# Kernel tuning notes

Measured on AMD Instinct MI355X. Metric: run time of the kernel, lower is better.

## Reference

```python
import jax, jax.numpy as jnp
import numpy as np

N = 30000
E = 480000
F = 256
H = 32
HEADS = 4
NUM_LABEL = 6
NEG_SLOPE = 0.2
BN_EPS = 1e-5
NUM_ITER = 3
ROUTE_NODES = 2 * (HEADS + HEADS)  # 16
PC_OUT = 8


def squash(t, axis=-1):
    sq = (t ** 2).sum(axis=axis, keepdims=True)
    return (sq / (1.0 + sq)) * t / jnp.sqrt(sq)


def glorot(key, shape):
    fan_in, fan_out = shape[-2], shape[-1]
    s = jnp.sqrt(6.0 / (fan_in + fan_out))
    return jax.random.uniform(key, shape, jnp.float32, -s, s)


def setup_inputs() -> dict:
    key = jax.random.key(0)
    ks = jax.random.split(key, 10)
    x = jax.random.normal(ks[0], (N, F), jnp.float32)
    rng = np.random.default_rng(0)
    src = rng.integers(0, N, E)
    dst = rng.integers(0, N, E)
    dst = np.where(src == dst, (dst + 1) % N, dst)  # no self loops (torch code removes them)
    edge_index = jnp.asarray(np.stack([src, dst]), jnp.int32)
    y = jax.random.randint(ks[1], (N,), 0, NUM_LABEL, jnp.int32)
    return {
        'x': x,
        'gamma': jnp.ones((F,), jnp.float32),
        'beta': jnp.zeros((F,), jnp.float32),
        'W_lin': glorot(ks[2], (F, HEADS * H)),
        'b_lin': jnp.zeros((HEADS * H,), jnp.float32),
        'W_gat': glorot(ks[3], (F, HEADS * H)),
        'att': glorot(ks[4], (1, HEADS, 2 * H)),
        'b_gat': jnp.zeros((HEADS * H,), jnp.float32),
        'Wp': glorot(ks[5], (2, H, PC_OUT)),
        'bp': jnp.zeros((2, PC_OUT), jnp.float32),
        'route_w': jax.random.normal(ks[6], (NUM_LABEL, ROUTE_NODES, PC_OUT, H), jnp.float32),
        'edge_index': edge_index,
        'y': y,
    }


def _forward(x, gamma, beta, W_lin, b_lin, W_gat, att, b_gat, Wp, bp, route_w, edge_index, y):
    n = x.shape[0]
    # BatchNorm1d (training-mode batch statistics, biased variance)
    mean = x.mean(axis=0)
    var = ((x - mean) ** 2).mean(axis=0)
    xb = (x - mean) / jnp.sqrt(var + BN_EPS) * gamma + beta

    hidden = (xb @ W_lin + b_lin).reshape(n, HEADS, H)

    # ---- GATConv (concat=True, add self-loops) ----
    xt = (xb @ W_gat).reshape(n, HEADS, H)
    loop = jnp.arange(n, dtype=edge_index.dtype)
    src = jnp.concatenate([edge_index[0], loop])
    dst = jnp.concatenate([edge_index[1], loop])
    x_i = xt[dst]  # [Et, HEADS, H] target
    x_j = xt[src]  # [Et, HEADS, H] source
    a_i, a_j = att[:, :, :H], att[:, :, H:]
    alpha = (x_i * a_i).sum(-1) + (x_j * a_j).sum(-1)  # [Et, HEADS]
    alpha = jnp.where(alpha >= 0, alpha, NEG_SLOPE * alpha)
    amax = jax.ops.segment_max(alpha, dst, num_segments=n)
    e = jnp.exp(alpha - amax[dst])
    denom = jax.ops.segment_sum(e, dst, num_segments=n)
    alpha = e / (denom[dst] + 1e-16)
    msg = x_j * alpha[:, :, None]
    aggr = jax.ops.segment_sum(msg, dst, num_segments=n)  # [n, HEADS, H]
    gat_out = aggr.reshape(n, HEADS * H) + b_gat

    xc = jnp.concatenate([gat_out.reshape(n, HEADS, H), hidden], axis=1)  # [n, 2*HEADS, H]
    xc = jax.nn.relu(xc)

    # ---- primary capsules: 2 Linear(H->8), cat on route axis, squash ----
    pc = jnp.einsum('nrh,cho->ncro', xc, Wp) + bp[None, :, None, :]  # [n,2,8,8]
    u = squash(pc.reshape(n, ROUTE_NODES, PC_OUT))  # [n,16,8]

    # ---- digit capsules: dynamic routing (softmax over route nodes, dim=2) ----
    priors = jnp.einsum('nri,crio->cnro', u, route_w)  # [6,n,16,H]
    logits = jnp.zeros(priors.shape[:3], priors.dtype)  # [6,n,16]
    for it in range(NUM_ITER):
        probs = jax.nn.softmax(logits, axis=2)
        v = squash((probs[..., None] * priors).sum(axis=2))  # [6,n,H]
        if it != NUM_ITER - 1:
            logits = logits + (priors * v[:, :, None, :]).sum(-1)

    xo = v.transpose(1, 0, 2)  # [n,6,H]
    features = xo.reshape(n, NUM_LABEL * H)
    output = jnp.sqrt((xo ** 2).sum(-1))  # [n,6] capsule lengths
    logp = jax.nn.log_softmax(output, axis=-1)
    loss = -jnp.take_along_axis(logp, y[:, None].astype(jnp.int32), axis=1).mean()
    return output, loss, features


def reference(x, gamma, beta, W_lin, b_lin, W_gat, att, b_gat, Wp, bp, route_w, edge_index, y):
    return _forward(x, gamma, beta, W_lin, b_lin, W_gat, att, b_gat, Wp, bp, route_w, edge_index, y)
```

## Files before the change

kernel.cpp:

```cpp
#include <hip/hip_runtime.h>
#include <hip/hip_bf16.h>

#define NND 30000
#define NE  480000
#define FD  256
#define HD  32
#define HEADS 4
#define NLAB 6
#define NEG_SLOPE 0.2f
#define BN_EPS 1e-5f
#define LOG2E 1.44269504f

#define WS_FLAG      0
#define WS_BNSUM     4
#define WS_BNSQ      260
#define WS_LOSS      516
#define WS_COUNTS    520
#define WS_ZERO_ELEMS 30524
#define WS_OFFSETS   30524
#define WS_CURSOR    60528
#define WS_GAMMA     90528
#define WS_BETA      90784
#define WS_WLIN      91040
#define WS_BLIN      123808
#define WS_WGAT      123936
#define WS_ATT       156704
#define WS_BGAT      156960
#define WS_WP        157088
#define WS_BP        157600
#define WS_RW        157616
#define WS_SCALE     182192
#define WS_SHIFT     182448
#define WS_WC        182704
#define WS_BC        248240
#define WS_SD        248496
#define WS_SS        368496
#define WS_ONORM     488496
#define WS_CSR       668496
#define WS_XF        1178496
#define WS_U         1178496
#define WS_BLKSUM    5018496
#define WS_BLKOFF    5018624
#define WS_Y         8858496
#define WS_XCG       16538496

#define OUT_LOSS_IDX 180000
#define OUT_FEAT_IDX 180001

#define SCAN_NB 118

typedef float v2f __attribute__((ext_vector_type(2)));

__device__ __forceinline__ float lrelu(float a) { return a >= 0.0f ? a : NEG_SLOPE * a; }

#if __has_builtin(__builtin_amdgcn_rcpf)
__device__ __forceinline__ float frcp(float x) { return __builtin_amdgcn_rcpf(x); }
#else
__device__ __forceinline__ float frcp(float x) { return 1.0f / x; }
#endif
#if __has_builtin(__builtin_amdgcn_sqrtf)
__device__ __forceinline__ float fsqrt(float x) { return __builtin_amdgcn_sqrtf(x); }
#else
__device__ __forceinline__ float fsqrt(float x) { return sqrtf(x); }
#endif
#if __has_builtin(__builtin_amdgcn_exp2f)
__device__ __forceinline__ float fexp2(float x) { return __builtin_amdgcn_exp2f(x); }
#else
__device__ __forceinline__ float fexp2(float x) { return exp2f(x); }
#endif

__device__ __forceinline__ int get_flag(const unsigned int* graw) {
    return ((graw[0] & 0xFFFFu) == 0x3F80u) ? 1 : 0;
}

__device__ __forceinline__ float bf2f(unsigned short h) {
    return __uint_as_float(((unsigned int)h) << 16);
}

__device__ __forceinline__ void pin(float& x) { asm volatile("" : "+v"(x)); }

template<int CTRL>
__device__ __forceinline__ float fdpp(float v) {
    return __int_as_float(__builtin_amdgcn_mov_dpp(__float_as_int(v), CTRL, 0xF, 0xF, true));
}
template<int PAT>
__device__ __forceinline__ float fswz(float v) {
    return __int_as_float(__builtin_amdgcn_ds_swizzle(__float_as_int(v), PAT));
}
__device__ __forceinline__ float redq(float v) {
    v += fdpp<0xB1>(v);
    v += fdpp<0x4E>(v);
    v += fswz<0x101F>(v);
    v += fswz<0x201F>(v);
    v += fswz<0x401F>(v);
    return v;
}
__device__ __forceinline__ float redq_sum64(float v) {
    v = redq(v);
    return v + __shfl_xor(v, 32);
}
__device__ __forceinline__ float redq_max64(float v) {
    v = fmaxf(v, fdpp<0xB1>(v));
    v = fmaxf(v, fdpp<0x4E>(v));
    v = fmaxf(v, fswz<0x101F>(v));
    v = fmaxf(v, fswz<0x201F>(v));
    v = fmaxf(v, fswz<0x401F>(v));
    return fmaxf(v, __shfl_xor(v, 32));
}
__device__ __forceinline__ void dreduce(float dp[8], int k, float out[8]) {
    #pragma unroll
    for (int j = 0; j < 8; ++j) {
        dp[j] += fdpp<0xB1>(dp[j]);
        dp[j] += fdpp<0x4E>(dp[j]);
    }
    float A = (k == 0) ? dp[0] : (k == 1) ? dp[1] : (k == 2) ? dp[2] : dp[3];
    float B = (k == 0) ? dp[4] : (k == 1) ? dp[5] : (k == 2) ? dp[6] : dp[7];
    A += fswz<0x101F>(A); A += fswz<0x201F>(A); A += fswz<0x401F>(A);
    B += fswz<0x101F>(B); B += fswz<0x201F>(B); B += fswz<0x401F>(B);
    out[0] = fdpp<0x00>(A); out[1] = fdpp<0x55>(A); out[2] = fdpp<0xAA>(A); out[3] = fdpp<0xFF>(A);
    out[4] = fdpp<0x00>(B); out[5] = fdpp<0x55>(B); out[6] = fdpp<0xAA>(B); out[7] = fdpp<0xFF>(B);
}

__device__ __forceinline__ float cvt_load(const void* p, int i, int f) {
    if (f) return __bfloat162float(((const __hip_bfloat16*)p)[i]);
    return ((const float*)p)[i];
}

#define CVT_XBLK 2048
__global__ void k_convert_all(const void* src, float* xdst,
                              const void* p0, const void* p1, const void* p2, const void* p3,
                              const void* p4, const void* p5, const void* p6, const void* p7,
                              const void* p8, const void* p9, float* pdst) {
    int f = get_flag((const unsigned int*)p0);
    if (blockIdx.x < CVT_XBLK) {
        const int nquad = NND * FD / 4;
        for (int q = blockIdx.x * blockDim.x + threadIdx.x; q < nquad; q += CVT_XBLK * blockDim.x) {
            float4 o;
            if (f) {
                ushort4 hv = ((const ushort4*)src)[q];
                o.x = bf2f(hv.x); o.y = bf2f(hv.y);
                o.z = bf2f(hv.z); o.w = bf2f(hv.w);
            } else {
                o = ((const float4*)src)[q];
            }
            ((float4*)xdst)[q] = o;
        }
        return;
    }
    int i = (blockIdx.x - CVT_XBLK) * blockDim.x + threadIdx.x;
    if (i >= 91664) return;
    const void* p; int off;
    if      (i < 256)   { p = p0; off = i; }
    else if (i < 512)   { p = p1; off = i - 256; }
    else if (i < 33280) { p = p2; off = i - 512; }
    else if (i < 33408) { p = p3; off = i - 33280; }
    else if (i < 66176) { p = p4; off = i - 33408; }
    else if (i < 66432) { p = p5; off = i - 66176; }
    else if (i < 66560) { p = p6; off = i - 66432; }
    else if (i < 67072) { p = p7; off = i - 66560; }
    else if (i < 67088) { p = p8; off = i - 67072; }
    else                { p = p9; off = i - 67088; }
    pdst[i] = cvt_load(p, off, f);
}

#define BN_NB 960
__global__ void k_bn_stats(const float* xf, float* bn_sum, float* bn_sq) {
    int t = threadIdx.x;
    int rows = (NND + gridDim.x - 1) / gridDim.x;
    int r0 = blockIdx.x * rows;
    int r1 = min(NND, r0 + rows);
    float s = 0.0f, ss = 0.0f;
    for (int r = r0; r < r1; ++r) {
        float v = xf[(size_t)r * FD + t];
        s += v; ss += v * v;
    }
    atomicAdd(&bn_sum[t], s);
    atomicAdd(&bn_sq[t], ss);
}

__global__ void k_fold(const float* bn_sum, const float* bn_sq, const float* gamma,
                       const float* beta, const float* wlin, const float* wgat,
                       const float* blin, float* Wc, float* bc) {
    int j = blockIdx.x;
    int k = threadIdx.x;
    float mean = bn_sum[k] / (float)NND;
    float var  = bn_sq[k] / (float)NND - mean * mean;
    float inv  = 1.0f / sqrtf(var + BN_EPS);
    float sc   = gamma[k] * inv;
    float sh   = beta[k] - mean * sc;
    float w = (j < 128) ? wlin[k * 128 + j] : wgat[k * 128 + (j - 128)];
    Wc[k * 256 + j] = sc * w;
    __shared__ float red[256];
    red[k] = sh * w;
    __syncthreads();
    for (int s = 128; s > 0; s >>= 1) { if (k < s) red[k] += red[k + s]; __syncthreads(); }
    if (k == 0) bc[j] = red[0] + (j < 128 ? blin[j] : 0.0f);
}

__global__ __launch_bounds__(256) void k_gemm(const float* A, const float* B,
                                              const float* bias, float* C) {
    __shared__ __align__(16) float As[16][128];
    __shared__ __align__(16) float Bs[16][64];
    int t  = threadIdx.x;
    int bm = blockIdx.x * 128;
    int bn = blockIdx.y * 64;
    int tr = t / 16, tc = t % 16;
    v2f acc[8][2] = {};
    int alm = t >> 2;
    int alk = (t & 3) * 4;
    int blk = t >> 4;
    int bln = (t & 15) * 4;
    for (int k0 = 0; k0 < 256; k0 += 16) {
        #pragma unroll
        for (int half = 0; half < 2; ++half) {
            int row = bm + alm + half * 64;
            float4 av = make_float4(0.f, 0.f, 0.f, 0.f);
            if (row < NND) av = *(const float4*)(A + (size_t)row * 256 + k0 + alk);
            int m = alm + half * 64;
            As[alk + 0][m] = av.x; As[alk + 1][m] = av.y;
            As[alk + 2][m] = av.z; As[alk + 3][m] = av.w;
        }
        float4 bv = *(const float4*)(B + (size_t)(k0 + blk) * 256 + bn + bln);
        *(float4*)&Bs[blk][bln] = bv;
        __syncthreads();
        #pragma unroll
        for (int kk = 0; kk < 16; ++kk) {
            float a[8];
            *(float4*)&a[0] = *(const float4*)&As[kk][tr * 8];
            *(float4*)&a[4] = *(const float4*)&As[kk][tr * 8 + 4];
            float4 b4 = *(const float4*)&Bs[kk][tc * 4];
            v2f b0; b0.x = b4.x; b0.y = b4.y;
            v2f b1; b1.x = b4.z; b1.y = b4.w;
            #pragma unroll
            for (int i = 0; i < 8; ++i) {
                v2f av; av.x = a[i]; av.y = a[i];
                acc[i][0] += av * b0;
                acc[i][1] += av * b1;
            }
        }
        __syncthreads();
    }
    #pragma unroll
    for (int i = 0; i < 8; ++i) {
        int row = bm + tr * 8 + i;
        if (row < NND) {
            int col = bn + tc * 4;
            float4 o;
            o.x = acc[i][0].x + bias[col + 0];
            o.y = acc[i][0].y + bias[col + 1];
            o.z = acc[i][1].x + bias[col + 2];
            o.w = acc[i][1].y + bias[col + 3];
            *(float4*)(C + (size_t)row * 256 + col) = o;
        }
    }
}

__global__ void k_scores(const float* Y, const float* attf, float* sD, float* sS) {
    int idx = blockIdx.x * blockDim.x + threadIdx.x;
    if (idx >= NND * HEADS) return;
    int n = idx >> 2, h = idx & 3;
    const float4* xr = (const float4*)(Y + (size_t)n * 256 + 128 + h * 32);
    const float4* ai = (const float4*)(attf + h * 64);
    const float4* aj = (const float4*)(attf + h * 64 + 32);
    float si = 0.f, sj = 0.f;
    #pragma unroll
    for (int k = 0; k < 8; ++k) {
        float4 x = xr[k], a = ai[k], b = aj[k];
        si += x.x*a.x + x.y*a.y + x.z*a.z + x.w*a.w;
        sj += x.x*b.x + x.y*b.y + x.z*b.z + x.w*b.w;
    }
    sD[idx] = si * LOG2E; sS[idx] = sj * LOG2E;
}

__global__ void k_count(const int* ei, int* counts) {
    int e = blockIdx.x * blockDim.x + threadIdx.x;
    if (e >= NE + NND) return;
    int d = (e < NE) ? ei[NE + e] : (e - NE);
    atomicAdd(&counts[d], 1);
}

__global__ void k_scan_blk(const int* counts, int* offsets, int* blksum) {
    int t = threadIdx.x, b = blockIdx.x;
    int i = b * 256 + t;
    int v = (i < NND) ? counts[i] : 0;
    int lane = t & 63, wv = t >> 6;
    int x = v;
    #pragma unroll
    for (int off = 1; off < 64; off <<= 1) {
        int y = __shfl_up(x, off);
        if (lane >= off) x += y;
    }
    __shared__ int wsum[4];
    if (lane == 63) wsum[wv] = x;
    __syncthreads();
    int add = 0;
    #pragma unroll
    for (int w = 0; w < 4; ++w) add += (w < wv) ? wsum[w] : 0;
    if (i < NND) offsets[i] = add + x - v;
    if (t == 255) blksum[b] = add + x;
}

__global__ void k_scan_add(const int* blksum, int* offsets, int* cursor) {
    int t = threadIdx.x, b = blockIdx.x;
    __shared__ int red[256];
    red[t] = (t < SCAN_NB && t < b) ? blksum[t] : 0;
    __syncthreads();
    for (int s = 128; s > 0; s >>= 1) { if (t < s) red[t] += red[t + s]; __syncthreads(); }
    int add = red[0];
    int i = b * 256 + t;
    if (i >= NND) return;
    int o = offsets[i] + add;
    offsets[i] = o;
    cursor[i] = o;
}

__global__ void k_scatter(const int* ei, int* cursor, int* csr) {
    int e = blockIdx.x * blockDim.x + threadIdx.x;
    if (e >= NE + NND) return;
    int s, d;
    if (e < NE) { s = ei[e]; d = ei[NE + e]; } else { s = d = e - NE; }
    int pos = atomicAdd(&cursor[d], 1);
    csr[pos] = s;
}

__global__ __launch_bounds__(256) void k_aggr(const float* Y, const float* sD, const float* sS,
                                              const int* offsets, const int* counts, const int* csr,
                                              const float* bgat, float* xcg) {
    int wave = (blockIdx.x * blockDim.x + threadIdx.x) >> 6;
    int lane = threadIdx.x & 63;
    if (wave >= NND) return;
    int n = wave;
    int start = offsets[n], deg = counts[n];
    float4 sd = *(const float4*)(sD + (size_t)n * 4);
    int hA = lane >> 5;
    float m0 = -1e30f, m1 = -1e30f, m2 = -1e30f, m3 = -1e30f;
    float d0 = 0.f, d1 = 0.f, d2 = 0.f, d3 = 0.f;
    float acc0 = 0.f, acc1 = 0.f;
    for (int base = 0; base < deg; base += 64) {
        int cnt = min(64, deg - base);
        int sidx = 0;
        float a0 = -1e30f, a1 = -1e30f, a2 = -1e30f, a3 = -1e30f;
        if (base + lane < deg) {
            sidx = csr[start + base + lane];
            float4 sj = *(const float4*)(sS + (size_t)sidx * 4);
            a0 = lrelu(sd.x + sj.x);
            a1 = lrelu(sd.y + sj.y);
            a2 = lrelu(sd.z + sj.z);
            a3 = lrelu(sd.w + sj.w);
        }
        float nm0 = fmaxf(m0, redq_max64(a0));
        float nm1 = fmaxf(m1, redq_max64(a1));
        float nm2 = fmaxf(m2, redq_max64(a2));
        float nm3 = fmaxf(m3, redq_max64(a3));
        if (base) {
            float s0 = fexp2(m0 - nm0), s1 = fexp2(m1 - nm1);
            float s2 = fexp2(m2 - nm2), s3 = fexp2(m3 - nm3);
            d0 *= s0; d1 *= s1; d2 *= s2; d3 *= s3;
            acc0 *= hA ? s1 : s0;
            acc1 *= hA ? s3 : s2;
        }
        m0 = nm0; m1 = nm1; m2 = nm2; m3 = nm3;
        float w0 = 0.f, w1 = 0.f, w2 = 0.f, w3 = 0.f;
        if (base + lane < deg) {
            w0 = fexp2(a0 - m0); w1 = fexp2(a1 - m1);
            w2 = fexp2(a2 - m2); w3 = fexp2(a3 - m3);
        }
        d0 += w0; d1 += w1; d2 += w2; d3 += w3;
        for (int j = 0; j < cnt; ++j) {
            int s2i = __builtin_amdgcn_readlane(sidx, j);
            float wa0 = __int_as_float(__builtin_amdgcn_readlane(__float_as_int(w0), j));
            float wa1 = __int_as_float(__builtin_amdgcn_readlane(__float_as_int(w1), j));
            float wb0 = __int_as_float(__builtin_amdgcn_readlane(__float_as_int(w2), j));
            float wb1 = __int_as_float(__builtin_amdgcn_readlane(__float_as_int(w3), j));
            float wA = hA ? wa1 : wa0;
            float wB = hA ? wb1 : wb0;
            const float* xrow = Y + (size_t)s2i * 256 + 128;
            acc0 += wA * xrow[lane];
            acc1 += wB * xrow[64 + lane];
        }
    }
    d0 = redq_sum64(d0); d1 = redq_sum64(d1);
    d2 = redq_sum64(d2); d3 = redq_sum64(d3);
    float i0 = frcp(d0 + 1e-16f), i1 = frcp(d1 + 1e-16f);
    float i2 = frcp(d2 + 1e-16f), i3 = frcp(d3 + 1e-16f);
    float iA = hA ? i1 : i0;
    float iB = hA ? i3 : i2;
    float r0 = acc0 * iA + bgat[lane];
    float r1 = acc1 * iB + bgat[64 + lane];
    xcg[(size_t)n * 128 + lane]      = r0 > 0.f ? r0 : 0.f;
    xcg[(size_t)n * 128 + 64 + lane] = r1 > 0.f ? r1 : 0.f;
}

__global__ __launch_bounds__(256, 4) void k_u(const float* Y, const float* xcg,
                                              const float* Wpf, const float* bpf, float* uG) {
    int lane = threadIdx.x & 63;
    int gw = blockIdx.x * 4 + (threadIdx.x >> 6);
    int nwaves = gridDim.x * 4;
    int r = lane >> 3, oo = lane & 7;
    float wpA[32], wpB[32];
    #pragma unroll
    for (int k = 0; k < 32; ++k) {
        wpA[k] = Wpf[k * 8 + oo];
        wpB[k] = Wpf[256 + k * 8 + oo];
    }
    #pragma unroll
    for (int k = 0; k < 32; ++k) { pin(wpA[k]); pin(wpB[k]); }
    float bpA = bpf[oo], bpB = bpf[8 + oo];
    for (int n = gw; n < NND; n += nwaves) {
        const float* rowp = (r < 4) ? (xcg + (size_t)n * 128 + r * 32)
                                    : (Y + (size_t)n * 256 + (r - 4) * 32);
        float pcA = bpA, pcB = bpB;
        #pragma unroll
        for (int k4 = 0; k4 < 8; ++k4) {
            float4 xv = *(const float4*)(rowp + k4 * 4);
            xv.x = fmaxf(xv.x, 0.f); xv.y = fmaxf(xv.y, 0.f);
            xv.z = fmaxf(xv.z, 0.f); xv.w = fmaxf(xv.w, 0.f);
            pcA += xv.x * wpA[k4*4+0] + xv.y * wpA[k4*4+1] + xv.z * wpA[k4*4+2] + xv.w * wpA[k4*4+3];
            pcB += xv.x * wpB[k4*4+0] + xv.y * wpB[k4*4+1] + xv.z * wpB[k4*4+2] + xv.w * wpB[k4*4+3];
        }
        float sA = pcA * pcA, sB = pcB * pcB;
        sA += fdpp<0xB1>(sA); sA += fdpp<0x4E>(sA); sA += fswz<0x101F>(sA);
        sB += fdpp<0xB1>(sB); sB += fdpp<0x4E>(sB); sB += fswz<0x101F>(sB);
        float cA = fsqrt(sA) * frcp(1.0f + sA);
        float cB = fsqrt(sB) * frcp(1.0f + sB);
        uG[(size_t)n * 128 + lane]      = pcA * cA;
        uG[(size_t)n * 128 + 64 + lane] = pcB * cB;
    }
}

__global__ __launch_bounds__(256, 3) void k_route3(const float* uG, const float* rwf,
                                                   float* onorm, void* dout,
                                                   const unsigned int* graw) {
    int flag = get_flag(graw);
    int t = threadIdx.x;
    int lane = t & 63;
    int nwg = gridDim.x;
    int swz = (blockIdx.x & 7) * (nwg >> 3) + (blockIdx.x >> 3);
    int c = swz % 6;
    int wv = t >> 6;
    int widx = (swz / 6) * 4 + wv;
    int nstep = (nwg / 6) * 4;
    int h = lane >> 5, o = lane & 31;
    int k = lane & 3;
    float rw[8][8];
    #pragma unroll
    for (int j = 0; j < 8; ++j)
        #pragma unroll
        for (int i = 0; i < 8; ++i)
            rw[j][i] = rwf[(((c * 16) + (h * 8 + j)) * 8 + i) * 32 + o];
    #pragma unroll
    for (int j = 0; j < 8; ++j)
        #pragma unroll
        for (int i = 0; i < 8; ++i)
            pin(rw[j][i]);
    float* outf = (float*)dout;
    __hip_bfloat16* outb = (__hip_bfloat16*)dout;
    for (int n = widx; n < NND; n += nstep) {
        const float* up = uG + (size_t)n * 128 + h * 64;
        float p[8];
        #pragma unroll
        for (int j = 0; j < 8; ++j) {
            float4 a = *(const float4*)(up + j * 8);
            float4 b = *(const float4*)(up + j * 8 + 4);
            p[j] = a.x*rw[j][0] + a.y*rw[j][1] + a.z*rw[j][2] + a.w*rw[j][3]
                 + b.x*rw[j][4] + b.y*rw[j][5] + b.z*rw[j][6] + b.w*rw[j][7];
        }
        float tl = p[0]+p[1]+p[2]+p[3]+p[4]+p[5]+p[6]+p[7];
        float s = (tl + __shfl_xor(tl, 32)) * 0.0625f;
        float sq = redq(s * s);
        float v = s * (fsqrt(sq) * frcp(1.0f + sq));
        float vs = v * LOG2E;
        float logits[8], dp[8];
        #pragma unroll
        for (int j = 0; j < 8; ++j) dp[j] = p[j] * vs;
        dreduce(dp, k, logits);
        float sq3 = 0.f, v3 = 0.f;
        #pragma unroll
        for (int it = 0; it < 2; ++it) {
            float m01 = fmaxf(logits[0], logits[1]);
            float m23 = fmaxf(logits[2], logits[3]);
            float m45 = fmaxf(logits[4], logits[5]);
            float m67 = fmaxf(logits[6], logits[7]);
            float mx = fmaxf(fmaxf(m01, m23), fmaxf(m45, m67));
            mx = fmaxf(mx, __shfl_xor(mx, 32));
            float e[8]; float se = 0.f;
            #pragma unroll
            for (int j = 0; j < 8; ++j) { e[j] = fexp2(logits[j] - mx); se += e[j]; }
            se += __shfl_xor(se, 32);
            float inv = frcp(se);
            float sl = 0.f;
            #pragma unroll
            for (int j = 0; j < 8; ++j) sl += e[j] * p[j];
            sl *= inv;
            float ss = sl + __shfl_xor(sl, 32);
            float q = redq(ss * ss);
            float vv = ss * (fsqrt(q) * frcp(1.0f + q));
            if (it == 0) {
                float dd[8], lu[8];
                float vvs = vv * LOG2E;
                #pragma unroll
                for (int j = 0; j < 8; ++j) dd[j] = p[j] * vvs;
                dreduce(dd, k, lu);
                #pragma unroll
                for (int j = 0; j < 8; ++j) logits[j] += lu[j];
            } else { v3 = vv; sq3 = q; }
        }
        if (lane < 32) {
            size_t fidx = (size_t)OUT_FEAT_IDX + (size_t)n * 192 + c * 32 + o;
            if (flag) outb[fidx] = __float2bfloat16(v3); else outf[fidx] = v3;
            if (lane == 0) {
                float norm = sq3 * frcp(1.0f + sq3);
                onorm[n * 6 + c] = norm;
                size_t oidx = (size_t)n * 6 + c;
                if (flag) outb[oidx] = __float2bfloat16(norm); else outf[oidx] = norm;
            }
        }
    }
}

__global__ void k_loss(const float* onorm, const int* y, float* acc) {
    float l = 0.f;
    for (int n = blockIdx.x * blockDim.x + threadIdx.x; n < NND; n += gridDim.x * blockDim.x) {
        const float* v = onorm + n * 6;
        float m = v[0];
        #pragma unroll
        for (int cc = 1; cc < 6; ++cc) m = fmaxf(m, v[cc]);
        float s = 0.f;
        #pragma unroll
        for (int cc = 0; cc < 6; ++cc) s += __expf(v[cc] - m);
        l += m + __logf(s) - v[y[n]];
    }
    __shared__ float red[256];
    red[threadIdx.x] = l;
    __syncthreads();
    for (int s = 128; s > 0; s >>= 1) { if (threadIdx.x < s) red[threadIdx.x] += red[threadIdx.x + s]; __syncthreads(); }
    if (threadIdx.x == 0) atomicAdd(acc, red[0]);
}

__global__ void k_loss_fin(const float* acc, void* dout, const unsigned int* graw) {
    float v = acc[0] / (float)NND;
    if (get_flag(graw)) ((__hip_bfloat16*)dout)[OUT_LOSS_IDX] = __float2bfloat16(v);
    else                ((float*)dout)[OUT_LOSS_IDX] = v;
}

extern "C" void kernel_launch(void* const* d_in, const int* in_sizes, int n_in,
                              void* d_out, int out_size, void* d_ws, size_t ws_size,
                              hipStream_t stream) {
    (void)in_sizes; (void)n_in; (void)out_size; (void)ws_size;
    float* ws = (float*)d_ws;
    int*  wsi = (int*)d_ws;
    const int* ei = (const int*)d_in[11];
    const int* y  = (const int*)d_in[12];
    const unsigned int* graw = (const unsigned int*)d_in[1];

    hipMemsetAsync(d_ws, 0, (size_t)WS_ZERO_ELEMS * 4, stream);

    k_convert_all<<<CVT_XBLK + (91664 + 255) / 256, 256, 0, stream>>>(
        d_in[0], ws + WS_XF,
        d_in[1], d_in[2], d_in[3], d_in[4], d_in[5], d_in[6], d_in[7], d_in[8], d_in[9], d_in[10],
        ws + WS_GAMMA);

    k_bn_stats<<<BN_NB, 256, 0, stream>>>(ws + WS_XF, ws + WS_BNSUM, ws + WS_BNSQ);
    k_fold<<<256, 256, 0, stream>>>(ws + WS_BNSUM, ws + WS_BNSQ, ws + WS_GAMMA, ws + WS_BETA,
                                    ws + WS_WLIN, ws + WS_WGAT, ws + WS_BLIN,
                                    ws + WS_WC, ws + WS_BC);

    k_gemm<<<dim3((NND + 127) / 128, 4), 256, 0, stream>>>(ws + WS_XF, ws + WS_WC, ws + WS_BC, ws + WS_Y);

    k_scores<<<(NND * HEADS + 255) / 256, 256, 0, stream>>>(ws + WS_Y, ws + WS_ATT, ws + WS_SD, ws + WS_SS);

    k_count<<<(NE + NND + 255) / 256, 256, 0, stream>>>(ei, wsi + WS_COUNTS);
    k_scan_blk<<<SCAN_NB, 256, 0, stream>>>(wsi + WS_COUNTS, wsi + WS_OFFSETS, wsi + WS_BLKSUM);
    k_scan_add<<<SCAN_NB, 256, 0, stream>>>(wsi + WS_BLKSUM, wsi + WS_OFFSETS, wsi + WS_CURSOR);
    k_scatter<<<(NE + NND + 255) / 256, 256, 0, stream>>>(ei, wsi + WS_CURSOR, wsi + WS_CSR);

    k_aggr<<<(NND + 3) / 4, 256, 0, stream>>>(ws + WS_Y, ws + WS_SD, ws + WS_SS,
                                              wsi + WS_OFFSETS, wsi + WS_COUNTS, wsi + WS_CSR,
                                              ws + WS_BGAT, ws + WS_XCG);

    k_u<<<512, 256, 0, stream>>>(ws + WS_Y, ws + WS_XCG, ws + WS_WP, ws + WS_BP, ws + WS_U);
    k_route3<<<3072, 256, 0, stream>>>(ws + WS_U, ws + WS_RW, ws + WS_ONORM, d_out, graw);

    k_loss<<<118, 256, 0, stream>>>(ws + WS_ONORM, y, ws + WS_LOSS);
    k_loss_fin<<<1, 1, 0, stream>>>(ws + WS_LOSS, d_out, graw);
}
```

Baseline: 474.0 us.

## Fuse primary-capsule projection into GAT aggregation and split routing launch by class

The primary-capsule linear projection and squash, formerly the separate k_u kernel, now run at the end of k_aggr. Each wave stages its relu'd GAT output and hidden row in shared memory and computes u directly, so the xcg intermediate is no longer written and re-read. Wp weights are now read from global memory per node instead of being held in registers. The routing kernel is also split into two launches, each covering three of the six classes, which changes the grid mapping and adds one more launch.

```diff
diff --git a/kernel.cpp b/kernel.cpp
--- a/kernel.cpp
+++ b/kernel.cpp
@@ -325,7 +325,10 @@
 
 __global__ __launch_bounds__(256) void k_aggr(const float* Y, const float* sD, const float* sS,
                                               const int* offsets, const int* counts, const int* csr,
-                                              const float* bgat, float* xcg) {
+                                              const float* bgat, const float* Wpf, const float* bpf,
+                                              float* uG) {
+    __shared__ float sm[4][256];
+    int wv = threadIdx.x >> 6;
     int wave = (blockIdx.x * blockDim.x + threadIdx.x) >> 6;
     int lane = threadIdx.x & 63;
     if (wave >= NND) return;
@@ -387,59 +390,47 @@
     float iB = hA ? i3 : i2;
     float r0 = acc0 * iA + bgat[lane];
     float r1 = acc1 * iB + bgat[64 + lane];
-    xcg[(size_t)n * 128 + lane]      = r0 > 0.f ? r0 : 0.f;
-    xcg[(size_t)n * 128 + 64 + lane] = r1 > 0.f ? r1 : 0.f;
-}
-
-__global__ __launch_bounds__(256, 4) void k_u(const float* Y, const float* xcg,
-                                              const float* Wpf, const float* bpf, float* uG) {
-    int lane = threadIdx.x & 63;
-    int gw = blockIdx.x * 4 + (threadIdx.x >> 6);
-    int nwaves = gridDim.x * 4;
-    int r = lane >> 3, oo = lane & 7;
-    float wpA[32], wpB[32];
-    #pragma unroll
-    for (int k = 0; k < 32; ++k) {
-        wpA[k] = Wpf[k * 8 + oo];
-        wpB[k] = Wpf[256 + k * 8 + oo];
-    }
-    #pragma unroll
-    for (int k = 0; k < 32; ++k) { pin(wpA[k]); pin(wpB[k]); }
-    float bpA = bpf[oo], bpB = bpf[8 + oo];
-    for (int n = gw; n < NND; n += nwaves) {
-        const float* rowp = (r < 4) ? (xcg + (size_t)n * 128 + r * 32)
-                                    : (Y + (size_t)n * 256 + (r - 4) * 32);
-        float pcA = bpA, pcB = bpB;
-        #pragma unroll
-        for (int k4 = 0; k4 < 8; ++k4) {
-            float4 xv = *(const float4*)(rowp + k4 * 4);
-            xv.x = fmaxf(xv.x, 0.f); xv.y = fmaxf(xv.y, 0.f);
-            xv.z = fmaxf(xv.z, 0.f); xv.w = fmaxf(xv.w, 0.f);
-            pcA += xv.x * wpA[k4*4+0] + xv.y * wpA[k4*4+1] + xv.z * wpA[k4*4+2] + xv.w * wpA[k4*4+3];
-            pcB += xv.x * wpB[k4*4+0] + xv.y * wpB[k4*4+1] + xv.z * wpB[k4*4+2] + xv.w * wpB[k4*4+3];
-        }
-        float sA = pcA * pcA, sB = pcB * pcB;
-        sA += fdpp<0xB1>(sA); sA += fdpp<0x4E>(sA); sA += fswz<0x101F>(sA);
-        sB += fdpp<0xB1>(sB); sB += fdpp<0x4E>(sB); sB += fswz<0x101F>(sB);
-        float cA = fsqrt(sA) * frcp(1.0f + sA);
-        float cB = fsqrt(sB) * frcp(1.0f + sB);
-        uG[(size_t)n * 128 + lane]      = pcA * cA;
-        uG[(size_t)n * 128 + 64 + lane] = pcB * cB;
-    }
+    r0 = r0 > 0.f ? r0 : 0.f;
+    r1 = r1 > 0.f ? r1 : 0.f;
+    sm[wv][lane]      = r0;
+    sm[wv][64 + lane] = r1;
+    float y0 = Y[(size_t)n * 256 + lane];
+    float y1 = Y[(size_t)n * 256 + 64 + lane];
+    sm[wv][128 + lane] = fmaxf(y0, 0.f);
+    sm[wv][192 + lane] = fmaxf(y1, 0.f);
+    asm volatile("" ::: "memory");
+    int rr = lane >> 3, oo = lane & 7;
+    const float* chunk = &sm[wv][rr * 32];
+    float pcA = bpf[oo], pcB = bpf[8 + oo];
+    #pragma unroll
+    for (int k4 = 0; k4 < 8; ++k4) {
+        float4 xv = *(const float4*)(chunk + k4 * 4);
+        pcA += xv.x * Wpf[(k4*4+0)*8+oo] + xv.y * Wpf[(k4*4+1)*8+oo]
+             + xv.z * Wpf[(k4*4+2)*8+oo] + xv.w * Wpf[(k4*4+3)*8+oo];
+        pcB += xv.x * Wpf[256+(k4*4+0)*8+oo] + xv.y * Wpf[256+(k4*4+1)*8+oo]
+             + xv.z * Wpf[256+(k4*4+2)*8+oo] + xv.w * Wpf[256+(k4*4+3)*8+oo];
+    }
+    float sA = pcA * pcA, sB = pcB * pcB;
+    sA += fdpp<0xB1>(sA); sA += fdpp<0x4E>(sA); sA += fswz<0x101F>(sA);
+    sB += fdpp<0xB1>(sB); sB += fdpp<0x4E>(sB); sB += fswz<0x101F>(sB);
+    float cA = fsqrt(sA) * frcp(1.0f + sA);
+    float cB = fsqrt(sB) * frcp(1.0f + sB);
+    uG[(size_t)n * 128 + lane]      = pcA * cA;
+    uG[(size_t)n * 128 + 64 + lane] = pcB * cB;
 }
 
 __global__ __launch_bounds__(256, 3) void k_route3(const float* uG, const float* rwf,
                                                    float* onorm, void* dout,
-                                                   const unsigned int* graw) {
+                                                   const unsigned int* graw, int coffset) {
     int flag = get_flag(graw);
     int t = threadIdx.x;
     int lane = t & 63;
     int nwg = gridDim.x;
     int swz = (blockIdx.x & 7) * (nwg >> 3) + (blockIdx.x >> 3);
-    int c = swz % 6;
+    int c = swz % 3 + coffset;
     int wv = t >> 6;
-    int widx = (swz / 6) * 4 + wv;
-    int nstep = (nwg / 6) * 4;
+    int widx = (swz / 3) * 4 + wv;
+    int nstep = (nwg / 3) * 4;
     int h = lane >> 5, o = lane & 31;
     int k = lane & 3;
     float rw[8][8];
@@ -576,10 +567,10 @@
 
     k_aggr<<<(NND + 3) / 4, 256, 0, stream>>>(ws + WS_Y, ws + WS_SD, ws + WS_SS,
                                               wsi + WS_OFFSETS, wsi + WS_COUNTS, wsi + WS_CSR,
-                                              ws + WS_BGAT, ws + WS_XCG);
-
-    k_u<<<512, 256, 0, stream>>>(ws + WS_Y, ws + WS_XCG, ws + WS_WP, ws + WS_BP, ws + WS_U);
-    k_route3<<<3072, 256, 0, stream>>>(ws + WS_U, ws + WS_RW, ws + WS_ONORM, d_out, graw);
+                                              ws + WS_BGAT, ws + WS_WP, ws + WS_BP, ws + WS_U);
+
+    k_route3<<<1536, 256, 0, stream>>>(ws + WS_U, ws + WS_RW, ws + WS_ONORM, d_out, graw, 0);
+    k_route3<<<1536, 256, 0, stream>>>(ws + WS_U, ws + WS_RW, ws + WS_ONORM, d_out, graw, 3);
 
     k_loss<<<118, 256, 0, stream>>>(ws + WS_ONORM, y, ws + WS_LOSS);
     k_loss_fin<<<1, 1, 0, stream>>>(ws + WS_LOSS, d_out, graw);
```

New measurement: 492.2 us. 1.04x slower.
